# Optimization experiments

Measured on AMD Instinct MI355X. Metric: run time of the kernel, lower is better.

The kernel has to match this reference:

```python
import jax, jax.numpy as jnp
import numpy as np

N_NODES = 100_000
N_EDGES = 1_600_000
D_IN = 64
D_HID = 64


def setup_inputs() -> dict:
    key = jax.random.key(0)
    ks = jax.random.split(key, 8)
    x = jax.random.normal(ks[0], (N_NODES, D_IN), dtype=jnp.float32)
    edge_index = jax.random.randint(ks[1], (2, N_EDGES), 0, N_NODES, dtype=jnp.int32)
    s = 1.0 / np.sqrt(D_IN)
    # PyG SAGEConv params per layer: lin_l (neighbor, with bias), lin_r (root, no bias)
    W1l = jax.random.uniform(ks[2], (D_HID, D_IN), jnp.float32, -s, s)
    b1 = jnp.zeros((D_HID,), jnp.float32)
    W1r = jax.random.uniform(ks[3], (D_HID, D_IN), jnp.float32, -s, s)
    s2 = 1.0 / np.sqrt(D_HID)
    W2l = jax.random.uniform(ks[4], (D_HID, D_HID), jnp.float32, -s2, s2)
    b2 = jnp.zeros((D_HID,), jnp.float32)
    W2r = jax.random.uniform(ks[5], (D_HID, D_HID), jnp.float32, -s2, s2)
    return {"x": x, "edge_index": edge_index, "W1l": W1l, "b1": b1, "W1r": W1r,
            "W2l": W2l, "b2": b2, "W2r": W2r}


def _sage_conv(x, src, dst, inv_deg, Wl, b, Wr):
    # mean-aggregate neighbor messages at destination nodes
    msg = jnp.take(x, src, axis=0)                       # [E, d] gather
    summed = jax.ops.segment_sum(msg, dst, num_segments=N_NODES)  # [N, d] scatter-add
    agg = summed * inv_deg                               # mean (0 for isolated nodes)
    return agg @ Wl.T + b + x @ Wr.T


def reference(x, edge_index, W1l, b1, W1r, W2l, b2, W2r):
    src, dst = edge_index[0], edge_index[1]
    deg = jax.ops.segment_sum(jnp.ones((N_EDGES,), x.dtype), dst, num_segments=N_NODES)
    inv_deg = (1.0 / jnp.maximum(deg, 1.0))[:, None]     # [N, 1]
    h = _sage_conv(x, src, dst, inv_deg, W1l, b1, W1r)
    h = jax.nn.relu(h)                                   # dropout = identity in eval
    h = _sage_conv(h, src, dst, inv_deg, W2l, b2, W2r)
    return h
```

## Files before the change

kernel.cpp:

```cpp
#include <hip/hip_runtime.h>


#define N_NODES 100000
#define N_EDGES 1600000
#define D 64
#define SLOT_CAP 48

#define B_SHIFT 9
#define NBKT ((N_NODES + (1 << B_SHIFT) - 1) >> B_SHIFT)
#define BUCKET_CAP 12288
#define P1_EDGES 2048
#define P1_GRID ((N_EDGES + P1_EDGES - 1) / P1_EDGES)

typedef unsigned int uint32;

__device__ __forceinline__ uint32 f2bf_rne(float f) {
    uint32 u = __float_as_uint(f);
    return (u + 0x7fffu + ((u >> 16) & 1u)) >> 16;
}

__global__ __launch_bounds__(256) void bucket_pass(const int* __restrict__ src,
                                                   const int* __restrict__ dst,
                                                   int* __restrict__ bcnt,
                                                   int* __restrict__ buf) {
    __shared__ int lcount[NBKT];
    __shared__ int lbase[NBKT];
    const int tid = threadIdx.x;
    for (int i = tid; i < NBKT; i += 256) lcount[i] = 0;
    __syncthreads();

    const int base = blockIdx.x * P1_EDGES;
    const int i0 = base + tid * 4;
    const int i1 = base + 1024 + tid * 4;
    const bool v0 = (i0 < N_EDGES);
    const bool v1 = (i1 < N_EDGES);
    int4 s0, d0, s1, d1;
    if (v0) { s0 = *(const int4*)(src + i0); d0 = *(const int4*)(dst + i0); }
    if (v1) { s1 = *(const int4*)(src + i1); d1 = *(const int4*)(dst + i1); }

    if (v0) {
        atomicAdd(&lcount[d0.x >> B_SHIFT], 1);
        atomicAdd(&lcount[d0.y >> B_SHIFT], 1);
        atomicAdd(&lcount[d0.z >> B_SHIFT], 1);
        atomicAdd(&lcount[d0.w >> B_SHIFT], 1);
    }
    if (v1) {
        atomicAdd(&lcount[d1.x >> B_SHIFT], 1);
        atomicAdd(&lcount[d1.y >> B_SHIFT], 1);
        atomicAdd(&lcount[d1.z >> B_SHIFT], 1);
        atomicAdd(&lcount[d1.w >> B_SHIFT], 1);
    }
    __syncthreads();
    for (int i = tid; i < NBKT; i += 256) {
        int c = lcount[i];
        lbase[i] = c ? atomicAdd(&bcnt[i], c) : 0;
        lcount[i] = 0;
    }
    __syncthreads();

#define PUT(S, DV)                                                     \
    {                                                                  \
        int b_ = (DV) >> B_SHIFT;                                      \
        int p_ = atomicAdd(&lcount[b_], 1) + lbase[b_];                \
        if (p_ < BUCKET_CAP)                                           \
            buf[b_ * BUCKET_CAP + p_] = (((DV) & 511) << 20) | (S);    \
    }
    if (v0) { PUT(s0.x, d0.x); PUT(s0.y, d0.y); PUT(s0.z, d0.z); PUT(s0.w, d0.w); }
    if (v1) { PUT(s1.x, d1.x); PUT(s1.y, d1.y); PUT(s1.z, d1.z); PUT(s1.w, d1.w); }
#undef PUT
}

#define P2_BLOCK 512
__global__ __launch_bounds__(P2_BLOCK) void slots_pass(const int* __restrict__ buf,
                                                       const int* __restrict__ bcnt,
                                                       int* __restrict__ cnt,
                                                       int* __restrict__ slots) {
    __shared__ int lcnt[1 << B_SHIFT];
    const int b = blockIdx.x;
    const int tid = threadIdx.x;
    for (int i = tid; i < (1 << B_SHIFT); i += P2_BLOCK) lcnt[i] = 0;
    __syncthreads();
    int count = bcnt[b];
    if (count > BUCKET_CAP) count = BUCKET_CAP;
    const int n0 = b << B_SHIFT;
    const int* eb = buf + b * BUCKET_CAP;
    for (int i = tid; i < count; i += P2_BLOCK) {
        int p = eb[i];
        int dl = ((unsigned)p) >> 20;
        int s = p & 0xFFFFF;
        int r = atomicAdd(&lcnt[dl], 1);
        if (r < SLOT_CAP) slots[(n0 + dl) * SLOT_CAP + r] = s;
    }
    __syncthreads();
    for (int j = tid; j < (1 << B_SHIFT); j += P2_BLOCK) {
        int node = n0 + j;
        if (node < N_NODES) cnt[node] = lcnt[j];
    }
}

#define GEMM_TM 128
#define PW 132
__global__ __launch_bounds__(256) void yz_gemm(const float* __restrict__ feat,
                                               const float* __restrict__ Wl,
                                               const float* __restrict__ Wr,
                                               const float* __restrict__ bias,
                                               uint32* __restrict__ ybf,
                                               float* __restrict__ z) {
    __shared__ float Ws[D][PW];
    __shared__ float As[D][PW];
    const int t = threadIdx.x;

    {
        int r = t & 127;
        int h = t >> 7;
        const float* wsrc = (r < D) ? &Wl[r * D] : &Wr[(r - D) * D];
#pragma unroll
        for (int q = 0; q < 8; ++q) {
            int k = h * 32 + q * 4;
            float4 v = *reinterpret_cast<const float4*>(&wsrc[k]);
            Ws[k + 0][r] = v.x; Ws[k + 1][r] = v.y;
            Ws[k + 2][r] = v.z; Ws[k + 3][r] = v.w;
        }
    }
    const int base = blockIdx.x * GEMM_TM;
#pragma unroll
    for (int p = 0; p < 8; ++p) {
        int n = p * 16 + (t >> 4);
        int node = base + n;
        if (node >= N_NODES) node = N_NODES - 1;
        int kk = (t & 15) * 4;
        float4 v = *reinterpret_cast<const float4*>(&feat[node * D + kk]);
        As[kk + 0][n] = v.x; As[kk + 1][n] = v.y;
        As[kk + 2][n] = v.z; As[kk + 3][n] = v.w;
    }
    __syncthreads();

    const int j0 = (t & 15) * 8;
    const int n0 = (t >> 4) * 8;
    float acc[8][8];
#pragma unroll
    for (int i = 0; i < 8; ++i)
#pragma unroll
        for (int j = 0; j < 8; ++j) acc[i][j] = 0.f;

#pragma unroll 4
    for (int k = 0; k < D; ++k) {
        float4 w0 = *reinterpret_cast<const float4*>(&Ws[k][j0]);
        float4 w1 = *reinterpret_cast<const float4*>(&Ws[k][j0 + 4]);
        float4 a0 = *reinterpret_cast<const float4*>(&As[k][n0]);
        float4 a1 = *reinterpret_cast<const float4*>(&As[k][n0 + 4]);
        float a[8] = {a0.x, a0.y, a0.z, a0.w, a1.x, a1.y, a1.z, a1.w};
        float w[8] = {w0.x, w0.y, w0.z, w0.w, w1.x, w1.y, w1.z, w1.w};
#pragma unroll
        for (int i = 0; i < 8; ++i)
#pragma unroll
            for (int j = 0; j < 8; ++j) acc[i][j] += a[i] * w[j];
    }

    if (j0 < D) {
#pragma unroll
        for (int i = 0; i < 8; ++i) {
            int node = base + n0 + i;
            if (node < N_NODES) {
                uint32 p0 = f2bf_rne(acc[i][0]) | (f2bf_rne(acc[i][1]) << 16);
                uint32 p1 = f2bf_rne(acc[i][2]) | (f2bf_rne(acc[i][3]) << 16);
                uint32 p2 = f2bf_rne(acc[i][4]) | (f2bf_rne(acc[i][5]) << 16);
                uint32 p3 = f2bf_rne(acc[i][6]) | (f2bf_rne(acc[i][7]) << 16);
                uint4 pk = make_uint4(p0, p1, p2, p3);
                *reinterpret_cast<uint4*>(&ybf[node * (D / 2) + (j0 >> 1)]) = pk;
            }
        }
    } else {
        const int zj = j0 - D;
        float bj[8];
#pragma unroll
        for (int j = 0; j < 8; ++j) bj[j] = bias[zj + j];
#pragma unroll
        for (int i = 0; i < 8; ++i) {
            int node = base + n0 + i;
            if (node < N_NODES) {
                float4 o0, o1;
                o0.x = acc[i][0] + bj[0]; o0.y = acc[i][1] + bj[1];
                o0.z = acc[i][2] + bj[2]; o0.w = acc[i][3] + bj[3];
                o1.x = acc[i][4] + bj[4]; o1.y = acc[i][5] + bj[5];
                o1.z = acc[i][6] + bj[6]; o1.w = acc[i][7] + bj[7];
                *reinterpret_cast<float4*>(&z[node * D + zj])     = o0;
                *reinterpret_cast<float4*>(&z[node * D + zj + 4]) = o1;
            }
        }
    }
}

template <int RELU>
__global__ __launch_bounds__(256, 8) void gather_mean(const uint32* __restrict__ ybf,
                                                      const float* __restrict__ z,
                                                      const int* __restrict__ slots,
                                                      const int* __restrict__ cnt,
                                                      float* __restrict__ out) {
    int node = blockIdx.x * 4 + (threadIdx.x >> 6);
    if (node >= N_NODES) return;
    const int lane = threadIdx.x & 63;
    const int half = lane >> 5;
    const int fp = lane & 31;
    int nodeu = __builtin_amdgcn_readfirstlane(node);
    int c = cnt[nodeu];
    float inv = 1.0f / fmaxf((float)c, 1.0f);
    int cc = (c > SLOT_CAP) ? SLOT_CAP : c;
    const int* sl = &slots[nodeu * SLOT_CAP];
    float2 zv = reinterpret_cast<const float2*>(z + nodeu * D)[fp];

    float ax[8], ay[8];
#pragma unroll
    for (int i = 0; i < 8; ++i) { ax[i] = 0.f; ay[i] = 0.f; }

    int k = 0;
    for (; k + 16 <= cc; k += 16) {
        int s[8];
#pragma unroll
        for (int i = 0; i < 8; ++i) s[i] = sl[k + 2 * i + half];
        uint32 v[8];
#pragma unroll
        for (int i = 0; i < 8; ++i) v[i] = ybf[s[i] * (D / 2) + fp];
#pragma unroll
        for (int i = 0; i < 8; ++i) {
            ax[i] += __uint_as_float(v[i] << 16);
            ay[i] += __uint_as_float(v[i] & 0xffff0000u);
        }
    }
    for (; k + 2 <= cc; k += 2) {
        int s = sl[k + half];
        uint32 v = ybf[s * (D / 2) + fp];
        ax[0] += __uint_as_float(v << 16);
        ay[0] += __uint_as_float(v & 0xffff0000u);
    }
    if (k < cc) {
        int s = sl[k];
        uint32 v = ybf[s * (D / 2) + fp];
        if (half == 0) {
            ax[1] += __uint_as_float(v << 16);
            ay[1] += __uint_as_float(v & 0xffff0000u);
        }
    }

    float sx = ((ax[0] + ax[4]) + (ax[1] + ax[5])) + ((ax[2] + ax[6]) + (ax[3] + ax[7]));
    float sy = ((ay[0] + ay[4]) + (ay[1] + ay[5])) + ((ay[2] + ay[6]) + (ay[3] + ay[7]));
    sx += __shfl_xor(sx, 32);
    sy += __shfl_xor(sy, 32);

    float2 o;
    o.x = zv.x + inv * sx;
    o.y = zv.y + inv * sy;
    if (RELU) { o.x = fmaxf(o.x, 0.f); o.y = fmaxf(o.y, 0.f); }
    if (half == 0)
        reinterpret_cast<float2*>(out + node * D)[fp] = o;
}

extern "C" void kernel_launch(void* const* d_in, const int* in_sizes, int n_in,
                              void* d_out, int out_size, void* d_ws, size_t ws_size,
                              hipStream_t stream) {
    const float* x   = (const float*)d_in[0];
    const int*   ei  = (const int*)d_in[1];
    const float* W1l = (const float*)d_in[2];
    const float* b1  = (const float*)d_in[3];
    const float* W1r = (const float*)d_in[4];
    const float* W2l = (const float*)d_in[5];
    const float* b2  = (const float*)d_in[6];
    const float* W2r = (const float*)d_in[7];
    float* out = (float*)d_out;

    const int* src = ei;
    const int* dst = ei + N_EDGES;

    char* ws = (char*)d_ws;
    int*    cnt   = (int*)ws;
    int*    slots = (int*)(ws + 400000);
    int*    bcnt  = (int*)(ws + 19600000);
    int*    buf   = (int*)(ws + 19600800);
    uint32* ybf   = (uint32*)(ws + 19600800);
    float*  z     = (float*)(ws + 19600800 + (size_t)N_NODES * (D / 2) * 4);
    float*  h1    = out;

    hipMemsetAsync(bcnt, 0, NBKT * 4, stream);
    bucket_pass<<<P1_GRID, 256, 0, stream>>>(src, dst, bcnt, buf);
    slots_pass<<<NBKT, P2_BLOCK, 0, stream>>>(buf, bcnt, cnt, slots);

    int gemm_grid   = (N_NODES + GEMM_TM - 1) / GEMM_TM;
    int gather_grid = (N_NODES + 3) / 4;

    yz_gemm<<<gemm_grid, 256, 0, stream>>>(x, W1l, W1r, b1, ybf, z);
    gather_mean<1><<<gather_grid, 256, 0, stream>>>(ybf, z, slots, cnt, h1);
    yz_gemm<<<gemm_grid, 256, 0, stream>>>(h1, W2l, W2r, b2, ybf, z);
    gather_mean<0><<<gather_grid, 256, 0, stream>>>(ybf, z, slots, cnt, out);
}
```

Measured before the change: 244.3 us.

## Split feature dimension into four planes and gather each plane separately

The bf16 projected features and the root term are stored as four column planes of 16 features each, and the neighbor-mean gather runs once per plane, so each pass's random-access working set is a quarter of the full table and can stay resident in cache. Inside the gather, each wave loads all slot indices at once, broadcasts them with shuffles, and handles 8 edges per round with 8 lanes per edge, reducing with xor shuffles. The cost is four times as many gather launches, four rereads of slots and counts, and a fixed 6-round loop that covers up to 48 edges even for nodes with few neighbors.

```diff
diff --git a/kernel.cpp b/kernel.cpp
--- a/kernel.cpp
+++ b/kernel.cpp
@@ -11,6 +11,11 @@
 #define BUCKET_CAP 12288
 #define P1_EDGES 2048
 #define P1_GRID ((N_EDGES + P1_EDGES - 1) / P1_EDGES)
+
+#define NPLANE 4
+#define PLANE_U 8
+#define PLANE_STRIDE ((size_t)N_NODES * PLANE_U)
+#define ZPLANE_STRIDE ((size_t)N_NODES * 16)
 
 typedef unsigned int uint32;
 
@@ -158,6 +163,9 @@
     }
 
     if (j0 < D) {
+        const int q = j0 >> 4;
+        const int u0 = (j0 >> 1) & 7;
+        uint32* yp = ybf + (size_t)q * PLANE_STRIDE;
 #pragma unroll
         for (int i = 0; i < 8; ++i) {
             int node = base + n0 + i;
@@ -166,12 +174,15 @@
                 uint32 p1 = f2bf_rne(acc[i][2]) | (f2bf_rne(acc[i][3]) << 16);
                 uint32 p2 = f2bf_rne(acc[i][4]) | (f2bf_rne(acc[i][5]) << 16);
                 uint32 p3 = f2bf_rne(acc[i][6]) | (f2bf_rne(acc[i][7]) << 16);
-                uint4 pk = make_uint4(p0, p1, p2, p3);
-                *reinterpret_cast<uint4*>(&ybf[node * (D / 2) + (j0 >> 1)]) = pk;
+                *reinterpret_cast<uint4*>(&yp[node * PLANE_U + u0]) =
+                    make_uint4(p0, p1, p2, p3);
             }
         }
     } else {
         const int zj = j0 - D;
+        const int q = zj >> 4;
+        const int off = zj & 15;
+        float* zp = z + (size_t)q * ZPLANE_STRIDE;
         float bj[8];
 #pragma unroll
         for (int j = 0; j < 8; ++j) bj[j] = bias[zj + j];
@@ -184,75 +195,56 @@
                 o0.z = acc[i][2] + bj[2]; o0.w = acc[i][3] + bj[3];
                 o1.x = acc[i][4] + bj[4]; o1.y = acc[i][5] + bj[5];
                 o1.z = acc[i][6] + bj[6]; o1.w = acc[i][7] + bj[7];
-                *reinterpret_cast<float4*>(&z[node * D + zj])     = o0;
-                *reinterpret_cast<float4*>(&z[node * D + zj + 4]) = o1;
+                *reinterpret_cast<float4*>(&zp[node * 16 + off])     = o0;
+                *reinterpret_cast<float4*>(&zp[node * 16 + off + 4]) = o1;
             }
         }
     }
 }
 
 template <int RELU>
-__global__ __launch_bounds__(256, 8) void gather_mean(const uint32* __restrict__ ybf,
-                                                      const float* __restrict__ z,
+__global__ __launch_bounds__(256, 8) void gather_mean(const uint32* __restrict__ plane,
+                                                      const float* __restrict__ zplane,
                                                       const int* __restrict__ slots,
                                                       const int* __restrict__ cnt,
-                                                      float* __restrict__ out) {
+                                                      float* __restrict__ out,
+                                                      int q) {
     int node = blockIdx.x * 4 + (threadIdx.x >> 6);
     if (node >= N_NODES) return;
     const int lane = threadIdx.x & 63;
-    const int half = lane >> 5;
-    const int fp = lane & 31;
+    const int u = lane & 7;
+    const int eg = lane >> 3;
     int nodeu = __builtin_amdgcn_readfirstlane(node);
     int c = cnt[nodeu];
     float inv = 1.0f / fmaxf((float)c, 1.0f);
     int cc = (c > SLOT_CAP) ? SLOT_CAP : c;
     const int* sl = &slots[nodeu * SLOT_CAP];
-    float2 zv = reinterpret_cast<const float2*>(z + nodeu * D)[fp];
-
-    float ax[8], ay[8];
-#pragma unroll
-    for (int i = 0; i < 8; ++i) { ax[i] = 0.f; ay[i] = 0.f; }
-
-    int k = 0;
-    for (; k + 16 <= cc; k += 16) {
-        int s[8];
-#pragma unroll
-        for (int i = 0; i < 8; ++i) s[i] = sl[k + 2 * i + half];
-        uint32 v[8];
-#pragma unroll
-        for (int i = 0; i < 8; ++i) v[i] = ybf[s[i] * (D / 2) + fp];
-#pragma unroll
-        for (int i = 0; i < 8; ++i) {
-            ax[i] += __uint_as_float(v[i] << 16);
-            ay[i] += __uint_as_float(v[i] & 0xffff0000u);
-        }
-    }
-    for (; k + 2 <= cc; k += 2) {
-        int s = sl[k + half];
-        uint32 v = ybf[s * (D / 2) + fp];
-        ax[0] += __uint_as_float(v << 16);
-        ay[0] += __uint_as_float(v & 0xffff0000u);
-    }
-    if (k < cc) {
-        int s = sl[k];
-        uint32 v = ybf[s * (D / 2) + fp];
-        if (half == 0) {
-            ax[1] += __uint_as_float(v << 16);
-            ay[1] += __uint_as_float(v & 0xffff0000u);
-        }
-    }
-
-    float sx = ((ax[0] + ax[4]) + (ax[1] + ax[5])) + ((ax[2] + ax[6]) + (ax[3] + ax[7]));
-    float sy = ((ay[0] + ay[4]) + (ay[1] + ay[5])) + ((ay[2] + ay[6]) + (ay[3] + ay[7]));
-    sx += __shfl_xor(sx, 32);
-    sy += __shfl_xor(sy, 32);
-
-    float2 o;
-    o.x = zv.x + inv * sx;
-    o.y = zv.y + inv * sy;
-    if (RELU) { o.x = fmaxf(o.x, 0.f); o.y = fmaxf(o.y, 0.f); }
-    if (half == 0)
-        reinterpret_cast<float2*>(out + node * D)[fp] = o;
+
+    float2 zv = make_float2(0.f, 0.f);
+    if (lane < 8) zv = *reinterpret_cast<const float2*>(&zplane[nodeu * 16 + 2 * u]);
+
+    int s_my = (lane < cc) ? sl[lane] : 0;
+
+    float ax = 0.f, ay = 0.f;
+#pragma unroll
+    for (int r = 0; r < 6; ++r) {
+        int k = r * 8 + eg;
+        int s = __shfl(s_my, k);
+        uint32 v = (k < cc) ? plane[(size_t)s * PLANE_U + u] : 0u;
+        ax += __uint_as_float(v << 16);
+        ay += __uint_as_float(v & 0xffff0000u);
+    }
+
+    ax += __shfl_xor(ax, 8); ax += __shfl_xor(ax, 16); ax += __shfl_xor(ax, 32);
+    ay += __shfl_xor(ay, 8); ay += __shfl_xor(ay, 16); ay += __shfl_xor(ay, 32);
+
+    if (lane < 8) {
+        float2 o;
+        o.x = zv.x + inv * ax;
+        o.y = zv.y + inv * ay;
+        if (RELU) { o.x = fmaxf(o.x, 0.f); o.y = fmaxf(o.y, 0.f); }
+        *reinterpret_cast<float2*>(&out[(size_t)node * D + q * 16 + 2 * u]) = o;
+    }
 }
 
 extern "C" void kernel_launch(void* const* d_in, const int* in_sizes, int n_in,
@@ -277,7 +269,7 @@
     int*    bcnt  = (int*)(ws + 19600000);
     int*    buf   = (int*)(ws + 19600800);
     uint32* ybf   = (uint32*)(ws + 19600800);
-    float*  z     = (float*)(ws + 19600800 + (size_t)N_NODES * (D / 2) * 4);
+    float*  z     = (float*)(ws + 32400800);
     float*  h1    = out;
 
     hipMemsetAsync(bcnt, 0, NBKT * 4, stream);
@@ -288,7 +280,13 @@
     int gather_grid = (N_NODES + 3) / 4;
 
     yz_gemm<<<gemm_grid, 256, 0, stream>>>(x, W1l, W1r, b1, ybf, z);
-    gather_mean<1><<<gather_grid, 256, 0, stream>>>(ybf, z, slots, cnt, h1);
+    for (int q = 0; q < NPLANE; ++q)
+        gather_mean<1><<<gather_grid, 256, 0, stream>>>(
+            ybf + (size_t)q * PLANE_STRIDE, z + (size_t)q * ZPLANE_STRIDE,
+            slots, cnt, h1, q);
     yz_gemm<<<gemm_grid, 256, 0, stream>>>(h1, W2l, W2r, b2, ybf, z);
-    gather_mean<0><<<gather_grid, 256, 0, stream>>>(ybf, z, slots, cnt, out);
-}
+    for (int q = 0; q < NPLANE; ++q)
+        gather_mean<0><<<gather_grid, 256, 0, stream>>>(
+            ybf + (size_t)q * PLANE_STRIDE, z + (size_t)q * ZPLANE_STRIDE,
+            slots, cnt, out, q);
+}
```

After: 315.0 us. +28.9%, slower.
